# Kernel optimization log

Measured on AMD Instinct MI355X. Metric: run time of the kernel, lower is better.

The kernel has to match this reference:

```python
import jax, jax.numpy as jnp
import numpy as np
import math

HC_MULT = 4
DIM = 32  # ENGRAM_DIM == HIDDEN_DIM == 32
EPS = float(jnp.finfo(jnp.float32).eps)  # torch RMSNorm default eps


def _rms_normalize(x):
    # x / sqrt(mean(x^2) + eps) over last dim
    ms = jnp.mean(x * x, axis=-1, keepdims=True)
    return x * jax.lax.rsqrt(ms + EPS)


def setup_inputs() -> dict:
    key = jax.random.key(0)
    ks = jax.random.split(key, 8)
    B, S = 16, 16384
    scale = 1.0 / math.sqrt(DIM)
    return {
        "embeddings": jax.random.normal(ks[0], (B, S, DIM), dtype=jnp.float32),
        "hidden_states": jax.random.normal(ks[1], (B, S, HC_MULT, DIM), dtype=jnp.float32),
        "Wv": jax.random.uniform(ks[2], (DIM, DIM), jnp.float32, -scale, scale),
        "bv": jax.random.uniform(ks[3], (DIM,), jnp.float32, -scale, scale),
        "Wk": jax.random.uniform(ks[4], (HC_MULT, DIM, DIM), jnp.float32, -scale, scale),
        "bk": jax.random.uniform(ks[5], (HC_MULT, DIM), jnp.float32, -scale, scale),
        "g1": jnp.ones((HC_MULT, DIM), jnp.float32),  # RMSNorm weights (norm1)
        "g2": jnp.ones((HC_MULT, DIM), jnp.float32),  # RMSNorm weights (norm2)
    }


def reference(embeddings, hidden_states, Wv, bv, Wk, bk, g1, g2):
    # keys for all heads at once: [B,S,H,K]
    key = jnp.einsum('bsd,hkd->bshk', embeddings, Wk) + bk
    normed_key = _rms_normalize(key) * g1  # g1 broadcasts [H,K]
    normed_query = _rms_normalize(hidden_states) * g2
    gate = jnp.sum(normed_key * normed_query, axis=-1) / math.sqrt(DIM)  # [B,S,H]
    gate = jnp.sqrt(jnp.maximum(jnp.abs(gate), 1e-6)) * jnp.sign(gate)
    gate = jax.nn.sigmoid(gate)[..., None]  # [B,S,H,1]
    value = (embeddings @ Wv.T + bv)[:, :, None, :]  # [B,S,1,K]
    return gate * value  # [B,S,H,K]
```

## Files before the change

### kernel.cpp

```cpp
#include <hip/hip_runtime.h>
#include <math.h>


#define GRID    2048
#define EPS32   3.814697265625e-06f
#define SQRT32  5.656854249492380f
#define LOG2E   1.4426950408889634f

#define DPP_ADD(x, ctrl) \
    x += __int_as_float(__builtin_amdgcn_update_dpp( \
        0, __float_as_int(x), ctrl, 0xF, 0xF, true))

__device__ __forceinline__ float half_sum_to_lane31(float x) {
    DPP_ADD(x, 0x111);
    DPP_ADD(x, 0x112);
    DPP_ADD(x, 0x114);
    DPP_ADD(x, 0x118);
    DPP_ADD(x, 0x142);
    return x;
}

__global__ __launch_bounds__(256) void engram_kernel(
    const float* __restrict__ emb,
    const float* __restrict__ hid,
    const float* __restrict__ Wv,
    const float* __restrict__ bv,
    const float* __restrict__ Wk,
    const float* __restrict__ bk,
    const float* __restrict__ g1,
    const float* __restrict__ g2,
    float* __restrict__ out,
    int ntok)
{
    __shared__ float Wl[16 * 160 * 2];
    __shared__ float Elds[4][8 * 32];

    const int tid  = threadIdx.x;
    const int wave = tid >> 6;
    const int lane = tid & 63;
    const int k    = lane & 31;
    const int h2   = lane >> 5;
    const int mytok = h2 * 4;

    for (int i = tid; i < 5120; i += 256) {
        int d = i & 31;
        int r = i >> 5;
        float v = (r < 128) ? Wk[r * 32 + d] : Wv[(r - 128) * 32 + d];
        Wl[(((d >> 1) * 160 + r) << 1) | (d & 1)] = v;
    }
    float bk_r[4], g12_r[4];
    #pragma unroll
    for (int h = 0; h < 4; ++h) {
        bk_r[h]  = bk[h * 32 + k];
        g12_r[h] = g1[h * 32 + k] * g2[h * 32 + k];
    }
    const float bv_r = bv[k];
    __syncthreads();

    const int tokens_per_block = ntok / GRID;
    const int iters = tokens_per_block >> 5;
    const int blk_base = blockIdx.x * tokens_per_block;
    const float2* __restrict__ W2 = (const float2*)Wl;

    for (int it = 0; it < iters; ++it) {
        const int tb = blk_base + it * 32 + wave * 8;

        {
            const float4 ev = *(const float4*)(emb + tb * 32 + lane * 4);
            *(float4*)&Elds[wave][lane * 4] = ev;
        }
        float q[4][4];
        #pragma unroll
        for (int t = 0; t < 4; ++t)
            #pragma unroll
            for (int h = 0; h < 4; ++h)
                q[t][h] = hid[(tb + mytok + t) * 128 + h * 32 + k];

        __asm__ volatile("s_waitcnt lgkmcnt(0)" ::: "memory");

        float kacc[4][4] = {{0.f,0.f,0.f,0.f},{0.f,0.f,0.f,0.f},
                            {0.f,0.f,0.f,0.f},{0.f,0.f,0.f,0.f}};
        float vacc[4] = {0.f, 0.f, 0.f, 0.f};

        #pragma unroll 8
        for (int dp = 0; dp < 16; ++dp) {
            const float2 w0 = W2[dp * 160 + k];
            const float2 w1 = W2[dp * 160 + 32 + k];
            const float2 w2 = W2[dp * 160 + 64 + k];
            const float2 w3 = W2[dp * 160 + 96 + k];
            const float2 wv = W2[dp * 160 + 128 + k];
            #pragma unroll
            for (int t = 0; t < 4; ++t) {
                const float2 e2 = *(const float2*)&Elds[wave][(mytok + t) * 32 + 2 * dp];
                kacc[t][0] = fmaf(e2.y, w0.y, fmaf(e2.x, w0.x, kacc[t][0]));
                kacc[t][1] = fmaf(e2.y, w1.y, fmaf(e2.x, w1.x, kacc[t][1]));
                kacc[t][2] = fmaf(e2.y, w2.y, fmaf(e2.x, w2.x, kacc[t][2]));
                kacc[t][3] = fmaf(e2.y, w3.y, fmaf(e2.x, w3.x, kacc[t][3]));
                vacc[t]    = fmaf(e2.y, wv.y, fmaf(e2.x, wv.x, vacc[t]));
            }
        }

        #pragma unroll
        for (int t = 0; t < 4; ++t) {
            vacc[t] += bv_r;
            float gate[4];
            #pragma unroll
            for (int h = 0; h < 4; ++h) {
                const float kk = kacc[t][h] + bk_r[h];
                float A  = kk * kk;
                float Bq = q[t][h] * q[t][h];
                float C  = kk * q[t][h] * g12_r[h];
                A  = half_sum_to_lane31(A);
                Bq = half_sum_to_lane31(Bq);
                C  = half_sum_to_lane31(C);
                float g = C * SQRT32 * __builtin_amdgcn_rsqf(A + EPS32)
                                     * __builtin_amdgcn_rsqf(Bq + EPS32);
                float r = copysignf(sqrtf(fmaxf(fabsf(g), 1e-6f)), g);
                float gl = 1.0f / (1.0f + __builtin_amdgcn_exp2f(-r * LOG2E));
                gate[h] = __int_as_float(
                    __builtin_amdgcn_ds_swizzle(__float_as_int(gl), 0x3FF));
            }
            const int ob = (tb + mytok + t) * 128 + k;
            #pragma unroll
            for (int h = 0; h < 4; ++h)
                out[ob + h * 32] = gate[h] * vacc[t];
        }
    }
}

extern "C" void kernel_launch(void* const* d_in, const int* in_sizes, int n_in,
                              void* d_out, int out_size, void* d_ws, size_t ws_size,
                              hipStream_t stream) {
    const float* emb = (const float*)d_in[0];
    const float* hid = (const float*)d_in[1];
    const float* Wv  = (const float*)d_in[2];
    const float* bv  = (const float*)d_in[3];
    const float* Wk  = (const float*)d_in[4];
    const float* bk  = (const float*)d_in[5];
    const float* g1  = (const float*)d_in[6];
    const float* g2  = (const float*)d_in[7];
    float* out = (float*)d_out;
    const int ntok = in_sizes[0] / 32;
    engram_kernel<<<GRID, 256, 0, stream>>>(emb, hid, Wv, bv, Wk, bk, g1, g2,
                                            out, ntok);
}
```

Baseline: 285.5 us.

## Transpose keys through LDS to compute gate reductions per lane instead of DPP

New measurement: 275.2 us. 1.04x faster.

```diff
diff --git a/kernel.cpp b/kernel.cpp
--- a/kernel.cpp
+++ b/kernel.cpp
@@ -6,19 +6,6 @@
 #define EPS32   3.814697265625e-06f
 #define SQRT32  5.656854249492380f
 #define LOG2E   1.4426950408889634f
-
-#define DPP_ADD(x, ctrl) \
-    x += __int_as_float(__builtin_amdgcn_update_dpp( \
-        0, __float_as_int(x), ctrl, 0xF, 0xF, true))
-
-__device__ __forceinline__ float half_sum_to_lane31(float x) {
-    DPP_ADD(x, 0x111);
-    DPP_ADD(x, 0x112);
-    DPP_ADD(x, 0x114);
-    DPP_ADD(x, 0x118);
-    DPP_ADD(x, 0x142);
-    return x;
-}
 
 __global__ __launch_bounds__(256) void engram_kernel(
     const float* __restrict__ emb,
@@ -32,8 +19,10 @@
     float* __restrict__ out,
     int ntok)
 {
-    __shared__ float Wl[16 * 160 * 2];
-    __shared__ float Elds[4][8 * 32];
+    __shared__ __align__(16) float Wl[16 * 160 * 2];
+    __shared__ __align__(16) float KL[4][32 * 32];
+    __shared__ __align__(16) float GL[4][32];
+    __shared__ __align__(16) float g12L[4 * 36];
 
     const int tid  = threadIdx.x;
     const int wave = tid >> 6;
@@ -48,14 +37,21 @@
         float v = (r < 128) ? Wk[r * 32 + d] : Wv[(r - 128) * 32 + d];
         Wl[(((d >> 1) * 160 + r) << 1) | (d & 1)] = v;
     }
-    float bk_r[4], g12_r[4];
+    if (tid < 128)
+        g12L[(tid >> 5) * 36 + (tid & 31)] = g1[tid] * g2[tid];
+
+    float bk_r[4];
     #pragma unroll
-    for (int h = 0; h < 4; ++h) {
-        bk_r[h]  = bk[h * 32 + k];
-        g12_r[h] = g1[h * 32 + k] * g2[h * 32 + k];
-    }
+    for (int h = 0; h < 4; ++h) bk_r[h] = bk[h * 32 + k];
     const float bv_r = bv[k];
     __syncthreads();
+
+    float* const KLw = KL[wave];
+    const int r2  = lane & 31;
+    const int kh  = lane >> 5;
+    const int t2  = r2 >> 2;
+    const int hh  = r2 & 3;
+    const int sw2 = r2 & 7;
 
     const int tokens_per_block = ntok / GRID;
     const int iters = tokens_per_block >> 5;
@@ -65,16 +61,15 @@
     for (int it = 0; it < iters; ++it) {
         const int tb = blk_base + it * 32 + wave * 8;
 
+        *(float4*)&KLw[lane * 4] = *(const float4*)(emb + tb * 32 + lane * 4);
+
+        float4 q4[4];
         {
-            const float4 ev = *(const float4*)(emb + tb * 32 + lane * 4);
-            *(float4*)&Elds[wave][lane * 4] = ev;
+            const float* qp = hid + (tb + t2) * 128 + hh * 32 + kh * 16;
+            #pragma unroll
+            for (int j = 0; j < 4; ++j)
+                q4[j] = *(const float4*)(qp + j * 4);
         }
-        float q[4][4];
-        #pragma unroll
-        for (int t = 0; t < 4; ++t)
-            #pragma unroll
-            for (int h = 0; h < 4; ++h)
-                q[t][h] = hid[(tb + mytok + t) * 128 + h * 32 + k];
 
         __asm__ volatile("s_waitcnt lgkmcnt(0)" ::: "memory");
 
@@ -91,7 +86,7 @@
             const float2 wv = W2[dp * 160 + 128 + k];
             #pragma unroll
             for (int t = 0; t < 4; ++t) {
-                const float2 e2 = *(const float2*)&Elds[wave][(mytok + t) * 32 + 2 * dp];
+                const float2 e2 = *(const float2*)&KLw[(mytok + t) * 32 + 2 * dp];
                 kacc[t][0] = fmaf(e2.y, w0.y, fmaf(e2.x, w0.x, kacc[t][0]));
                 kacc[t][1] = fmaf(e2.y, w1.y, fmaf(e2.x, w1.x, kacc[t][1]));
                 kacc[t][2] = fmaf(e2.y, w2.y, fmaf(e2.x, w2.x, kacc[t][2]));
@@ -100,30 +95,63 @@
             }
         }
 
+        {
+            const int cblk = k >> 2, ksub = k & 3;
+            #pragma unroll
+            for (int t = 0; t < 4; ++t) {
+                #pragma unroll
+                for (int h = 0; h < 4; ++h) {
+                    const int row = h2 * 16 + t * 4 + h;
+                    KLw[row * 32 + (((cblk ^ (row & 7)) << 2) | ksub)] =
+                        kacc[t][h] + bk_r[h];
+                }
+            }
+        }
+        #pragma unroll
+        for (int t = 0; t < 4; ++t) vacc[t] += bv_r;
+
+        __asm__ volatile("s_waitcnt lgkmcnt(0)" ::: "memory");
+
+        float A = 0.f, Bq = 0.f, C = 0.f;
+        #pragma unroll
+        for (int j = 0; j < 4; ++j) {
+            const int cblk = kh * 4 + j;
+            const float4 kk4 = *(const float4*)&KLw[r2 * 32 + ((cblk ^ sw2) << 2)];
+            const float4 g4  = *(const float4*)&g12L[hh * 36 + kh * 16 + j * 4];
+            const float4 q   = q4[j];
+            A  = fmaf(kk4.x, kk4.x, A);
+            A  = fmaf(kk4.y, kk4.y, A);
+            A  = fmaf(kk4.z, kk4.z, A);
+            A  = fmaf(kk4.w, kk4.w, A);
+            Bq = fmaf(q.x, q.x, Bq);
+            Bq = fmaf(q.y, q.y, Bq);
+            Bq = fmaf(q.z, q.z, Bq);
+            Bq = fmaf(q.w, q.w, Bq);
+            C  = fmaf(kk4.x, q.x * g4.x, C);
+            C  = fmaf(kk4.y, q.y * g4.y, C);
+            C  = fmaf(kk4.z, q.z * g4.z, C);
+            C  = fmaf(kk4.w, q.w * g4.w, C);
+        }
+        A  += __shfl_xor(A, 32);
+        Bq += __shfl_xor(Bq, 32);
+        C  += __shfl_xor(C, 32);
+
+        float g = C * SQRT32 * __builtin_amdgcn_rsqf(A + EPS32)
+                             * __builtin_amdgcn_rsqf(Bq + EPS32);
+        float rr = copysignf(sqrtf(fmaxf(fabsf(g), 1e-6f)), g);
+        float gl = 1.0f / (1.0f + __builtin_amdgcn_exp2f(-rr * LOG2E));
+        if (kh == 0) GL[wave][r2] = gl;
+
+        __asm__ volatile("s_waitcnt lgkmcnt(0)" ::: "memory");
+
+        const int ob = (tb + mytok) * 128 + k;
         #pragma unroll
         for (int t = 0; t < 4; ++t) {
-            vacc[t] += bv_r;
-            float gate[4];
-            #pragma unroll
-            for (int h = 0; h < 4; ++h) {
-                const float kk = kacc[t][h] + bk_r[h];
-                float A  = kk * kk;
-                float Bq = q[t][h] * q[t][h];
-                float C  = kk * q[t][h] * g12_r[h];
-                A  = half_sum_to_lane31(A);
-                Bq = half_sum_to_lane31(Bq);
-                C  = half_sum_to_lane31(C);
-                float g = C * SQRT32 * __builtin_amdgcn_rsqf(A + EPS32)
-                                     * __builtin_amdgcn_rsqf(Bq + EPS32);
-                float r = copysignf(sqrtf(fmaxf(fabsf(g), 1e-6f)), g);
-                float gl = 1.0f / (1.0f + __builtin_amdgcn_exp2f(-r * LOG2E));
-                gate[h] = __int_as_float(
-                    __builtin_amdgcn_ds_swizzle(__float_as_int(gl), 0x3FF));
-            }
-            const int ob = (tb + mytok + t) * 128 + k;
-            #pragma unroll
-            for (int h = 0; h < 4; ++h)
-                out[ob + h * 32] = gate[h] * vacc[t];
+            const float4 gt = *(const float4*)&GL[wave][h2 * 16 + t * 4];
+            out[ob + t * 128]      = gt.x * vacc[t];
+            out[ob + t * 128 + 32] = gt.y * vacc[t];
+            out[ob + t * 128 + 64] = gt.z * vacc[t];
+            out[ob + t * 128 + 96] = gt.w * vacc[t];
         }
     }
 }
```

## Keep Wk in registers, split the d-reduction across half-waves, and vectorize gate reductions

Applied to the files above, without the earlier changes.

Measured after the change: 320.3 us. +12.2%, slower.

```diff
diff --git a/kernel.cpp b/kernel.cpp
--- a/kernel.cpp
+++ b/kernel.cpp
@@ -7,18 +7,17 @@
 #define SQRT32  5.656854249492380f
 #define LOG2E   1.4426950408889634f
 
-#define DPP_ADD(x, ctrl) \
-    x += __int_as_float(__builtin_amdgcn_update_dpp( \
-        0, __float_as_int(x), ctrl, 0xF, 0xF, true))
-
-__device__ __forceinline__ float half_sum_to_lane31(float x) {
-    DPP_ADD(x, 0x111);
-    DPP_ADD(x, 0x112);
-    DPP_ADD(x, 0x114);
-    DPP_ADD(x, 0x118);
-    DPP_ADD(x, 0x142);
-    return x;
+__device__ __forceinline__ float xsum32(float x) {
+    return x + __shfl_xor(x, 32);
 }
+__device__ __forceinline__ float xadd16(float x) {
+    return x + __int_as_float(
+        __builtin_amdgcn_ds_swizzle(__float_as_int(x), 0x401F));
+}
+#define FENCE() do { \
+    __asm__ volatile("s_waitcnt lgkmcnt(0)" ::: "memory"); \
+    __builtin_amdgcn_sched_barrier(0); \
+} while (0)
 
 __global__ __launch_bounds__(256) void engram_kernel(
     const float* __restrict__ emb,
@@ -32,98 +31,141 @@
     float* __restrict__ out,
     int ntok)
 {
-    __shared__ float Wl[16 * 160 * 2];
-    __shared__ float Elds[4][8 * 32];
+    __shared__ __align__(16) float KL[4][16 * 32];
+    __shared__ __align__(16) float EST[4][128];
+    __shared__ __align__(16) float WvL[16 * 32 * 2];
+    __shared__ __align__(16) float GL[4][16];
+    __shared__ __align__(16) float g12L[4 * 36];
+    __shared__ float bkL[160];
 
     const int tid  = threadIdx.x;
     const int wave = tid >> 6;
     const int lane = tid & 63;
     const int k    = lane & 31;
     const int h2   = lane >> 5;
-    const int mytok = h2 * 4;
 
-    for (int i = tid; i < 5120; i += 256) {
-        int d = i & 31;
-        int r = i >> 5;
-        float v = (r < 128) ? Wk[r * 32 + d] : Wv[(r - 128) * 32 + d];
-        Wl[(((d >> 1) * 160 + r) << 1) | (d & 1)] = v;
+    for (int i = tid; i < 512; i += 256) {
+        const int dp = i >> 5, kk = i & 31;
+        ((float2*)WvL)[i] = make_float2(Wv[kk * 32 + 2 * dp],
+                                        Wv[kk * 32 + 2 * dp + 1]);
     }
-    float bk_r[4], g12_r[4];
+    if (tid < 128) g12L[(tid >> 5) * 36 + (tid & 31)] = g1[tid] * g2[tid];
+    if (tid < 160) bkL[tid] = (tid < 128) ? bk[tid] : bv[tid - 128];
+
+    float2 Wr[4][8];
     #pragma unroll
-    for (int h = 0; h < 4; ++h) {
-        bk_r[h]  = bk[h * 32 + k];
-        g12_r[h] = g1[h * 32 + k] * g2[h * 32 + k];
-    }
-    const float bv_r = bv[k];
+    for (int ch = 0; ch < 4; ++ch)
+        #pragma unroll
+        for (int dp = 0; dp < 8; ++dp)
+            Wr[ch][dp] = *(const float2*)(Wk + (ch * 32 + k) * 32
+                                             + h2 * 16 + 2 * dp);
     __syncthreads();
 
-    const int tokens_per_block = ntok / GRID;
-    const int iters = tokens_per_block >> 5;
-    const int blk_base = blockIdx.x * tokens_per_block;
-    const float2* __restrict__ W2 = (const float2*)Wl;
+    float* const KLw  = KL[wave];
+    float* const ESTw = EST[wave];
+    const float2* const WvL2 = (const float2*)WvL;
+
+    const int row = lane & 15;
+    const int kq  = lane >> 4;
+    const int t2  = row >> 2;
+    const int hh  = row & 3;
+    const int sw  = row & 7;
+
+    const int tpb   = ntok / GRID;
+    const int iters = tpb >> 4;
+    const int blk   = blockIdx.x * tpb;
+
+    float2 ereg = *(const float2*)(emb + (blk + wave * 4) * 32 + lane * 2);
 
     for (int it = 0; it < iters; ++it) {
-        const int tb = blk_base + it * 32 + wave * 8;
+        const int tb = blk + it * 16 + wave * 4;
 
+        *(float2*)&ESTw[lane * 2] = ereg;
         {
-            const float4 ev = *(const float4*)(emb + tb * 32 + lane * 4);
-            *(float4*)&Elds[wave][lane * 4] = ev;
+            const int ntb = (it + 1 < iters) ? tb + 16 : tb;
+            ereg = *(const float2*)(emb + ntb * 32 + lane * 2);
         }
-        float q[4][4];
+        FENCE();
+
+        float2 ka[4][4] = {};
+        float  va[4]    = {0.f, 0.f, 0.f, 0.f};
+
         #pragma unroll
-        for (int t = 0; t < 4; ++t)
-            #pragma unroll
-            for (int h = 0; h < 4; ++h)
-                q[t][h] = hid[(tb + mytok + t) * 128 + h * 32 + k];
-
-        __asm__ volatile("s_waitcnt lgkmcnt(0)" ::: "memory");
-
-        float kacc[4][4] = {{0.f,0.f,0.f,0.f},{0.f,0.f,0.f,0.f},
-                            {0.f,0.f,0.f,0.f},{0.f,0.f,0.f,0.f}};
-        float vacc[4] = {0.f, 0.f, 0.f, 0.f};
-
-        #pragma unroll 8
-        for (int dp = 0; dp < 16; ++dp) {
-            const float2 w0 = W2[dp * 160 + k];
-            const float2 w1 = W2[dp * 160 + 32 + k];
-            const float2 w2 = W2[dp * 160 + 64 + k];
-            const float2 w3 = W2[dp * 160 + 96 + k];
-            const float2 wv = W2[dp * 160 + 128 + k];
+        for (int dp = 0; dp < 8; ++dp) {
+            const float2 wv = WvL2[(h2 * 8 + dp) * 32 + k];
             #pragma unroll
             for (int t = 0; t < 4; ++t) {
-                const float2 e2 = *(const float2*)&Elds[wave][(mytok + t) * 32 + 2 * dp];
-                kacc[t][0] = fmaf(e2.y, w0.y, fmaf(e2.x, w0.x, kacc[t][0]));
-                kacc[t][1] = fmaf(e2.y, w1.y, fmaf(e2.x, w1.x, kacc[t][1]));
-                kacc[t][2] = fmaf(e2.y, w2.y, fmaf(e2.x, w2.x, kacc[t][2]));
-                kacc[t][3] = fmaf(e2.y, w3.y, fmaf(e2.x, w3.x, kacc[t][3]));
-                vacc[t]    = fmaf(e2.y, wv.y, fmaf(e2.x, wv.x, vacc[t]));
+                const float2 e2 = *(const float2*)&ESTw[t * 32 + h2 * 16 + 2 * dp];
+                #pragma unroll
+                for (int ch = 0; ch < 4; ++ch) {
+                    ka[t][ch].x = fmaf(e2.x, Wr[ch][dp].x, ka[t][ch].x);
+                    ka[t][ch].y = fmaf(e2.y, Wr[ch][dp].y, ka[t][ch].y);
+                }
+                va[t] = fmaf(e2.x, wv.x, fmaf(e2.y, wv.y, va[t]));
             }
         }
 
+        const float* qp = hid + (tb + t2) * 128 + hh * 32 + kq * 8;
+        const float4 qa = *(const float4*)qp;
+        const float4 qb = *(const float4*)(qp + 4);
+
+        float ks[4][4], vs[4];
         #pragma unroll
         for (int t = 0; t < 4; ++t) {
-            vacc[t] += bv_r;
-            float gate[4];
             #pragma unroll
-            for (int h = 0; h < 4; ++h) {
-                const float kk = kacc[t][h] + bk_r[h];
-                float A  = kk * kk;
-                float Bq = q[t][h] * q[t][h];
-                float C  = kk * q[t][h] * g12_r[h];
-                A  = half_sum_to_lane31(A);
-                Bq = half_sum_to_lane31(Bq);
-                C  = half_sum_to_lane31(C);
-                float g = C * SQRT32 * __builtin_amdgcn_rsqf(A + EPS32)
-                                     * __builtin_amdgcn_rsqf(Bq + EPS32);
-                float r = copysignf(sqrtf(fmaxf(fabsf(g), 1e-6f)), g);
-                float gl = 1.0f / (1.0f + __builtin_amdgcn_exp2f(-r * LOG2E));
-                gate[h] = __int_as_float(
-                    __builtin_amdgcn_ds_swizzle(__float_as_int(gl), 0x3FF));
+            for (int ch = 0; ch < 4; ++ch)
+                ks[t][ch] = xsum32(ka[t][ch].x + ka[t][ch].y) + bkL[ch * 32 + k];
+            vs[t] = xsum32(va[t]) + bkL[128 + k];
+        }
+
+        {
+            const int cblk = k >> 2, ksub = k & 3;
+            #pragma unroll
+            for (int j = 0; j < 2; ++j) {
+                #pragma unroll
+                for (int h = 0; h < 4; ++h) {
+                    const int r = (h2 * 2 + j) * 4 + h;
+                    const float val = h2 ? ks[2 + j][h] : ks[j][h];
+                    KLw[r * 32 + (((cblk ^ (r & 7)) << 2) | ksub)] = val;
+                }
             }
-            const int ob = (tb + mytok + t) * 128 + k;
-            #pragma unroll
-            for (int h = 0; h < 4; ++h)
-                out[ob + h * 32] = gate[h] * vacc[t];
+        }
+        FENCE();
+
+        float A = 0.f, Bq = 0.f, C = 0.f;
+        #pragma unroll
+        for (int c = 0; c < 2; ++c) {
+            const int cb = kq * 2 + c;
+            const float4 kk4 = *(const float4*)&KLw[row * 32 + ((cb ^ sw) << 2)];
+            const float4 g4  = *(const float4*)&g12L[hh * 36 + cb * 4];
+            const float4 q   = c ? qb : qa;
+            A  = fmaf(kk4.w, kk4.w, fmaf(kk4.z, kk4.z,
+                 fmaf(kk4.y, kk4.y, fmaf(kk4.x, kk4.x, A))));
+            Bq = fmaf(q.w, q.w, fmaf(q.z, q.z,
+                 fmaf(q.y, q.y, fmaf(q.x, q.x, Bq))));
+            C  = fmaf(kk4.w, q.w * g4.w, fmaf(kk4.z, q.z * g4.z,
+                 fmaf(kk4.y, q.y * g4.y, fmaf(kk4.x, q.x * g4.x, C))));
+        }
+        A  = xsum32(xadd16(A));
+        Bq = xsum32(xadd16(Bq));
+        C  = xsum32(xadd16(C));
+
+        const float g  = C * SQRT32 * __builtin_amdgcn_rsqf(A + EPS32)
+                                    * __builtin_amdgcn_rsqf(Bq + EPS32);
+        const float rr = copysignf(sqrtf(fmaxf(fabsf(g), 1e-6f)), g);
+        const float gl = 1.0f / (1.0f + __builtin_amdgcn_exp2f(-rr * LOG2E));
+        if (lane < 16) GL[wave][row] = gl;
+        FENCE();
+
+        #pragma unroll
+        for (int j = 0; j < 2; ++j) {
+            const float  vv = h2 ? vs[2 + j] : vs[j];
+            const float4 gt = *(const float4*)&GL[wave][(h2 * 2 + j) * 4];
+            const int    ob = (tb + h2 * 2 + j) * 128 + k;
+            out[ob]      = gt.x * vv;
+            out[ob + 32] = gt.y * vv;
+            out[ob + 64] = gt.z * vv;
+            out[ob + 96] = gt.w * vv;
         }
     }
 }
```
